# Kernel optimization log

Measured on AMD Instinct MI355X. Metric: run time of the kernel, lower is better.

Reference implementation:

```python
import math
import jax, jax.numpy as jnp
import numpy as np

B, S, D_IN, D_OUT = 8, 4096, 512, 512
CHUNK = 64
MAX_LR = 0.2        # config.max_memory_lr
MIN_DECAY = 0.5     # config.min_memory_decay
MAX_NORM = 30.0     # config.memory_max_norm
NORM_EPS = 1e-5     # config.norm_eps (used in normalize_for_delta)


def setup_inputs() -> dict:
    key = jax.random.key(0)
    ks = jax.random.split(key, 5)
    x = jax.random.normal(ks[0], (B, S, D_IN), dtype=jnp.float32)
    # M_init: xavier_uniform(gain=0.1) ~ small; use small normal
    M_init = jax.random.normal(ks[1], (D_OUT, D_IN), dtype=jnp.float32) * 0.02
    # hyperparam projections (Linear(d_in, 1)); torch init: zero weight, logit bias.
    # Use small random weights so the data-dependent path is exercised.
    eta_w = jax.random.normal(ks[2], (1, D_IN), dtype=jnp.float32) * 0.01
    eta_b = jnp.full((1,), math.log(0.08 / 0.92), dtype=jnp.float32)   # inv_sig(memory_lr_init)
    alpha_w = jax.random.normal(ks[3], (1, D_IN), dtype=jnp.float32) * 0.01
    alpha_b = jnp.full((1,), math.log(0.85 / 0.15), dtype=jnp.float32)  # inv_sig(memory_decay_init)
    gate_w = jax.random.normal(ks[4], (1, D_IN), dtype=jnp.float32) * 0.01
    gate_b = jnp.full((1,), 2.0, dtype=jnp.float32)
    return {"x": x, "M_init": M_init, "eta_w": eta_w, "eta_b": eta_b,
            "alpha_w": alpha_w, "alpha_b": alpha_b, "gate_w": gate_w, "gate_b": gate_b}


def _forward(x, M_init, eta_w, eta_b, alpha_w, alpha_b, gate_w, gate_b):
    n_chunks = S // CHUNK
    # [n_chunks, B, C, d_in] for scan over chunks
    xc = x.reshape(B, n_chunks, CHUNK, D_IN).transpose(1, 0, 2, 3)
    M0 = jnp.broadcast_to(M_init, (B, D_OUT, D_IN))

    def step(M, chunk):  # M: [B, d_out, d_in], chunk: [B, C, d_in]
        # per-chunk hyperparams (training mode: base logits = 0)
        eta_tok = jax.nn.sigmoid(chunk @ eta_w.T + eta_b) * MAX_LR            # [B,C,1]
        alpha_tok = MIN_DECAY + jax.nn.sigmoid(chunk @ alpha_w.T + alpha_b) * (1.0 - MIN_DECAY)
        eta = eta_tok.mean(axis=1, keepdims=True)    # [B,1,1]
        alpha = alpha_tok.mean(axis=1, keepdims=True)
        # retrieval: chunk @ M^T
        outputs = jnp.einsum('bcd,bod->bco', chunk, M)  # [B,C,d_out]
        # normalized keys (F.normalize: x / max(||x||, eps))
        kn = jnp.linalg.norm(chunk, axis=-1, keepdims=True)
        keys = chunk / jnp.maximum(kn, NORM_EPS)
        k_mean = keys.mean(axis=1)        # [B,d_in]
        v_target = outputs.mean(axis=1)   # [B,d_out]
        # delta rule rank-1 update
        Mk = jnp.einsum('bod,bd->bo', M, k_mean)
        error = v_target - Mk
        update = error[:, :, None] * k_mean[:, None, :]  # [B,d_out,d_in]
        # chunk_scale = min(C/chunk_size, 1) = 1 here
        M_new = alpha * M + eta * update
        gate = jax.nn.sigmoid(k_mean @ gate_w.T + gate_b)[:, :, None]  # [B,1,1]
        M_new = gate * M_new + (1.0 - gate) * M
        # frobenius-norm clamp
        M_norm = jnp.sqrt(jnp.sum(M_new * M_new, axis=(-2, -1), keepdims=True))
        scale = jnp.minimum(MAX_NORM / (M_norm + 1e-6), 1.0)
        return M_new * scale, outputs

    M_fin, outs = jax.lax.scan(step, M0, xc)  # outs: [n_chunks,B,C,d_out]
    out = outs.transpose(1, 0, 2, 3).reshape(B, S, D_OUT)
    return out, M_fin


def reference(x, M_init, eta_w, eta_b, alpha_w, alpha_b, gate_w, gate_b):
    return _forward(x, M_init, eta_w, eta_b, alpha_w, alpha_b, gate_w, gate_b)
```

## Files before the change

### kernel.cpp

```cpp
#include <hip/hip_runtime.h>
#include <math.h>

#define DIN  512
#define DOUT 512
#define CHK  64
#define NCH  64
#define NB   8
#define SEQ  4096

typedef short bh8_t __attribute__((ext_vector_type(8)));
typedef float f32x4 __attribute__((ext_vector_type(4)));

__device__ __forceinline__ float sigmoidf_(float z){ return 1.0f/(1.0f+__expf(-z)); }

__device__ __forceinline__ unsigned short f2bf(float f){
  unsigned u = __float_as_uint(f);
  unsigned r = (u + 0x7fffu + ((u>>16)&1u)) >> 16;
  return (unsigned short)r;
}
__device__ __forceinline__ void store_bf4(unsigned short* p, float4 v){
  uint2 u;
  u.x = (unsigned)f2bf(v.x) | ((unsigned)f2bf(v.y)<<16);
  u.y = (unsigned)f2bf(v.z) | ((unsigned)f2bf(v.w)<<16);
  *(uint2*)p = u;
}

__global__ __launch_bounds__(256) void k0_m0h(const float* __restrict__ M0, unsigned short* __restrict__ M0h){
  int idx = (blockIdx.x*256 + threadIdx.x)*4;
  float4 v = *(const float4*)(M0+idx);
  store_bf4(M0h+idx, v);
}

__global__ __launch_bounds__(256) void k1_stats(
    const float* __restrict__ x,
    const float* __restrict__ eta_w, const float* __restrict__ eta_b,
    const float* __restrict__ alpha_w, const float* __restrict__ alpha_b,
    const float* __restrict__ gate_w, const float* __restrict__ gate_b,
    float* __restrict__ KM, float* __restrict__ Dv, unsigned short* __restrict__ KMh,
    float* __restrict__ C1, float* __restrict__ C2, float* __restrict__ KM2, float* __restrict__ Q,
    unsigned short* __restrict__ xh)
{
  int j = blockIdx.x, b = blockIdx.y;
  const float* xc = x + ((size_t)b*SEQ + (size_t)j*CHK) * DIN;
  int tid = threadIdx.x;
  int wave = tid >> 6, lane = tid & 63;

  float km_acc[8], xb_acc[8];
#pragma unroll
  for (int k=0;k<8;k++){ km_acc[k]=0.f; xb_acc[k]=0.f; }
  float eta_sum = 0.f, alpha_sum = 0.f;
  float ew[8], aw[8];
#pragma unroll
  for (int k=0;k<8;k++){ ew[k]=eta_w[lane*8+k]; aw[k]=alpha_w[lane*8+k]; }

  for (int tt=0; tt<16; tt++){
    int t = wave*16 + tt;
    const float* xr = xc + (size_t)t*DIN + lane*8;
    float v[8];
#pragma unroll
    for (int k=0;k<8;k++) v[k]=xr[k];
    if (xh){
      uint4 hv;
      hv.x = (unsigned)f2bf(v[0]) | ((unsigned)f2bf(v[1])<<16);
      hv.y = (unsigned)f2bf(v[2]) | ((unsigned)f2bf(v[3])<<16);
      hv.z = (unsigned)f2bf(v[4]) | ((unsigned)f2bf(v[5])<<16);
      hv.w = (unsigned)f2bf(v[6]) | ((unsigned)f2bf(v[7])<<16);
      *(uint4*)&xh[((size_t)b*SEQ + (size_t)j*CHK + t)*DIN + lane*8] = hv;
    }
    float pe=0.f, pa=0.f, pn=0.f;
#pragma unroll
    for (int k=0;k<8;k++){ pe += v[k]*ew[k]; pa += v[k]*aw[k]; pn += v[k]*v[k]; }
#pragma unroll
    for (int off=32; off; off>>=1){
      pe += __shfl_xor(pe, off);
      pa += __shfl_xor(pa, off);
      pn += __shfl_xor(pn, off);
    }
    float inv = 1.0f / fmaxf(sqrtf(pn), 1e-5f);
    eta_sum   += sigmoidf_(pe + eta_b[0]);
    alpha_sum += sigmoidf_(pa + alpha_b[0]);
#pragma unroll
    for (int k=0;k<8;k++){ km_acc[k] += v[k]*inv; xb_acc[k] += v[k]; }
  }

  __shared__ float sKM[4][DIN];
  __shared__ float sXB[4][DIN];
  __shared__ float sEA[4][2];
  __shared__ float sred[4][2];
#pragma unroll
  for (int k=0;k<8;k++){ sKM[wave][lane*8+k]=km_acc[k]; sXB[wave][lane*8+k]=xb_acc[k]; }
  if (lane==0){ sEA[wave][0]=eta_sum; sEA[wave][1]=alpha_sum; }
  __syncthreads();

  float gpart=0.f, km2part=0.f;
  float kmv[2], dvv[2];
#pragma unroll
  for (int k=0;k<2;k++){
    int d = tid*2+k;
    float km = (sKM[0][d]+sKM[1][d]+sKM[2][d]+sKM[3][d]) * (1.0f/64.0f);
    float xb = (sXB[0][d]+sXB[1][d]+sXB[2][d]+sXB[3][d]) * (1.0f/64.0f);
    kmv[k]=km; dvv[k]=xb-km;
    gpart  += km * gate_w[d];
    km2part+= km * km;
  }
#pragma unroll
  for (int off=32; off; off>>=1){
    gpart   += __shfl_xor(gpart, off);
    km2part += __shfl_xor(km2part, off);
  }
  if (lane==0){ sred[wave][0]=gpart; sred[wave][1]=km2part; }
  __syncthreads();

  size_t base = ((size_t)b*NCH + j)*DIN;
#pragma unroll
  for (int k=0;k<2;k++){
    int d = tid*2+k;
    KM[base+d]=kmv[k];
    Dv[base+d]=dvv[k];
    KMh[base+d]=f2bf(kmv[k]);
  }
  if (tid==0){
    float gdot = sred[0][0]+sred[1][0]+sred[2][0]+sred[3][0];
    float km2  = sred[0][1]+sred[1][1]+sred[2][1]+sred[3][1];
    float etam = (sEA[0][0]+sEA[1][0]+sEA[2][0]+sEA[3][0]) * (1.0f/64.0f);
    float alpm = (sEA[0][1]+sEA[1][1]+sEA[2][1]+sEA[3][1]) * (1.0f/64.0f);
    float eta   = 0.2f * etam;
    float alpha = 0.5f + 0.5f * alpm;
    float gate  = sigmoidf_(gdot + gate_b[0]);
    float c1 = gate*alpha + 1.0f - gate;
    float c2 = gate*eta;
    C1[b*NCH+j]  = c1;
    C2[b*NCH+j]  = c2;
    KM2[b*NCH+j] = km2;
    Q[b*NCH+j]   = c2/c1;
  }
}

__global__ __launch_bounds__(256) void k2_g0h0(
    const float* __restrict__ KM, const float* __restrict__ Dv,
    const float* __restrict__ M0, float* __restrict__ G0, float* __restrict__ H0)
{
  int j = blockIdx.x, b = blockIdx.y, half = blockIdx.z;
  __shared__ float sD[DIN], sK[DIN];
  int tid = threadIdx.x;
  size_t base = ((size_t)b*NCH+j)*DIN;
  for (int d=tid; d<DIN; d+=256){ sD[d]=Dv[base+d]; sK[d]=KM[base+d]; }
  __syncthreads();
  int o = half*256 + tid;
  const float* mr = M0 + (size_t)o*DIN;
  float ag=0.f, ah=0.f;
  for (int d=0; d<DIN; d+=4){
    float4 m = *(const float4*)(mr+d);
    ag += m.x*sD[d] + m.y*sD[d+1] + m.z*sD[d+2] + m.w*sD[d+3];
    ah += m.x*sK[d] + m.y*sK[d+1] + m.z*sK[d+2] + m.w*sK[d+3];
  }
  G0[base+o]=ag; H0[base+o]=ah;
}

__global__ __launch_bounds__(512) void k2b_gram(
    const float* __restrict__ KM, const float* __restrict__ Dv,
    const float* __restrict__ Q,
    float* __restrict__ GT, float* __restrict__ WT)
{
  int i = blockIdx.x, b = blockIdx.y;
  __shared__ float sKi[DIN];
  int tid = threadIdx.x;
  const float* kmi = KM + ((size_t)b*NCH+i)*DIN;
  for (int d=tid; d<DIN; d+=512) sKi[d]=kmi[d];
  __syncthreads();
  float qi = Q[b*NCH+i];
  int wave = tid>>6, lane = tid&63;
  for (int j=wave; j<NCH; j+=8){
    const float* dj = Dv + ((size_t)b*NCH+j)*DIN;
    const float* kj = KM + ((size_t)b*NCH+j)*DIN;
    float pd=0.f, pk=0.f;
#pragma unroll
    for (int k=0;k<8;k++){
      int d = lane + k*64;
      pd += sKi[d]*dj[d];
      pk += sKi[d]*kj[d];
    }
#pragma unroll
    for (int off=32; off; off>>=1){ pd += __shfl_xor(pd,off); pk += __shfl_xor(pk,off); }
    if (lane==0){
      GT[((size_t)b*NCH+j)*NCH + i] = qi*pd;
      WT[((size_t)b*NCH+j)*NCH + i] = qi*pk;
    }
  }
}

__global__ __launch_bounds__(64) void k3a_rec(
    const float* __restrict__ G0, const float* __restrict__ H0,
    const float* __restrict__ GT, const float* __restrict__ WT,
    const float* __restrict__ Q,
    float* __restrict__ AU, unsigned short* __restrict__ UQTh, float* __restrict__ DOTS)
{
  int dblk = blockIdx.x, b = blockIdx.y;
  int lane = threadIdx.x;
  int d = dblk*64 + lane;

  __shared__ float sMT[NCH*NCH];
  __shared__ float sWT[NCH*NCH];
  __shared__ float sq[NCH];

  const float4* gt4 = (const float4*)&GT[(size_t)b*NCH*NCH];
  const float4* wt4 = (const float4*)&WT[(size_t)b*NCH*NCH];
#pragma unroll
  for (int t=0;t<16;t++){
    int idx4 = t*64 + lane;
    int idx  = idx4*4;
    int j = idx>>6, i0 = idx&63;
    float4 g = gt4[idx4];
    float4 w = wt4[idx4];
    if (i0+0 >= j){ g.x=0.f; w.x=0.f; }
    if (i0+1 >= j){ g.y=0.f; w.y=0.f; }
    if (i0+2 >= j){ g.z=0.f; w.z=0.f; }
    if (i0+3 >= j){ g.w=0.f; w.w=0.f; }
    *(float4*)&sMT[idx] = g;
    *(float4*)&sWT[idx] = w;
  }
  sq[lane] = Q[b*NCH+lane];
  __syncthreads();

  float au[NCH];
  size_t gb = (size_t)b*NCH*DOUT + d;
#pragma unroll
  for (int j=0;j<NCH;j++) au[j] = G0[gb + (size_t)j*DOUT];

#pragma unroll
  for (int j=1;j<NCH;j++){
    float a = au[j];
    const f32x4* row = (const f32x4*)&sMT[j*64];
    int ng = (j+3)>>2;
#pragma unroll
    for (int g=0; g<ng; g++){
      f32x4 c = row[g];
      a += c[0]*au[g*4+0] + c[1]*au[g*4+1] + c[2]*au[g*4+2] + c[3]*au[g*4+3];
    }
    au[j] = a;
  }
#pragma unroll
  for (int j=0;j<NCH;j++) AU[gb + (size_t)j*DOUT] = au[j];

#pragma unroll
  for (int g=0; g<8; g++){
    uint4 hv;
    hv.x = (unsigned)f2bf(au[g*8+0]*sq[g*8+0]) | ((unsigned)f2bf(au[g*8+1]*sq[g*8+1])<<16);
    hv.y = (unsigned)f2bf(au[g*8+2]*sq[g*8+2]) | ((unsigned)f2bf(au[g*8+3]*sq[g*8+3])<<16);
    hv.z = (unsigned)f2bf(au[g*8+4]*sq[g*8+4]) | ((unsigned)f2bf(au[g*8+5]*sq[g*8+5])<<16);
    hv.w = (unsigned)f2bf(au[g*8+6]*sq[g*8+6]) | ((unsigned)f2bf(au[g*8+7]*sq[g*8+7])<<16);
    *(uint4*)&UQTh[((size_t)b*DOUT + d)*NCH + g*8] = hv;
  }

#pragma unroll
  for (int j=0;j<NCH;j++){
    float w = H0[gb + (size_t)j*DOUT];
    const f32x4* row = (const f32x4*)&sWT[j*64];
    int ng = (j+3)>>2;
#pragma unroll
    for (int g=0; g<ng; g++){
      f32x4 c = row[g];
      w += c[0]*au[g*4+0] + c[1]*au[g*4+1] + c[2]*au[g*4+2] + c[3]*au[g*4+3];
    }
    float s1 = au[j]*w, s2 = au[j]*au[j];
#pragma unroll
    for (int off=32; off; off>>=1){ s1+=__shfl_xor(s1,off); s2+=__shfl_xor(s2,off); }
    if (lane==0){
      DOTS[(((size_t)b*8+dblk)*NCH+j)*2+0] = s1;
      DOTS[(((size_t)b*8+dblk)*NCH+j)*2+1] = s2;
    }
  }
}

__global__ __launch_bounds__(256) void k3b_chain(
    const float* __restrict__ M0, const float* __restrict__ DOTS,
    const float* __restrict__ C1, const float* __restrict__ C2, const float* __restrict__ KM2,
    float* __restrict__ P)
{
  int b = blockIdx.x;
  int tid = threadIdx.x, wave = tid>>6, lane = tid&63;
  __shared__ float sF[4];
  __shared__ float suw[NCH], suu[NCH], sc1[NCH], sc2[NCH], skm2[NCH];

  float f0p = 0.f;
  const float4* m4 = (const float4*)M0;
  for (int i=tid; i<(DOUT*DIN)/4; i+=256){
    float4 v = m4[i];
    f0p += v.x*v.x + v.y*v.y + v.z*v.z + v.w*v.w;
  }
#pragma unroll
  for (int off=32; off; off>>=1) f0p += __shfl_xor(f0p, off);
  if (lane==0) sF[wave]=f0p;

  if (tid < NCH){
    float uw=0.f, uu=0.f;
#pragma unroll
    for (int k=0;k<8;k++){
      uw += DOTS[(((size_t)b*8+k)*NCH+tid)*2+0];
      uu += DOTS[(((size_t)b*8+k)*NCH+tid)*2+1];
    }
    suw[tid]=uw; suu[tid]=uu;
    sc1[tid]=C1[b*NCH+tid]; sc2[tid]=C2[b*NCH+tid]; skm2[tid]=KM2[b*NCH+tid];
  }
  __syncthreads();

  if (tid==0){
    float F = sF[0]+sF[1]+sF[2]+sF[3];
    float p = 1.f;
    P[b*65+0] = 1.f;
    for (int j=0;j<NCH;j++){
      float uw = suw[j], uu = suu[j];
      float c1 = sc1[j], c2 = sc2[j], km2 = skm2[j];
      uw *= p*p; uu *= p*p;
      float Fnew = c1*c1*F + 2.f*c1*c2*uw + c2*c2*uu*km2;
      float scale = fminf(30.0f/(sqrtf(Fnew)+1e-6f), 1.0f);
      F = scale*scale*Fnew;
      p = scale*c1*p;
      P[b*65+j+1] = p;
    }
  }
}

__global__ __launch_bounds__(256) void k4s_s(
    const float* __restrict__ x, const unsigned short* __restrict__ xh,
    const unsigned short* __restrict__ KMh,
    unsigned short* __restrict__ Sh, int use_xh)
{
  int tt = blockIdx.x, b = blockIdx.y;
  int tid = threadIdx.x;
  int lane = tid&63, w = tid>>6, m = lane&15, q = lane>>4;
  __shared__ unsigned short As[64*72];
  __shared__ unsigned short Bs[64*72];
  f32x4 acc[4];
  f32x4 z = {0.f,0.f,0.f,0.f};
#pragma unroll
  for (int nf=0;nf<4;nf++) acc[nf]=z;

  for (int k0=0;k0<DIN;k0+=64){
    uint4 bb[2];
#pragma unroll
    for (int v=0;v<2;v++){
      int idx=v*256+tid; int il=idx>>3, cc=idx&7;
      bb[v] = *(const uint4*)&KMh[((size_t)b*NCH+il)*DIN + k0 + cc*8];
    }
    if (use_xh){
      uint4 av[2];
#pragma unroll
      for (int v=0;v<2;v++){
        int idx=v*256+tid; int row=idx>>3, cc=idx&7;
        av[v] = *(const uint4*)&xh[((size_t)b*SEQ + (size_t)tt*64 + row)*DIN + k0 + cc*8];
      }
      __syncthreads();
#pragma unroll
      for (int v=0;v<2;v++){
        int idx=v*256+tid; int row=idx>>3, cc=idx&7;
        *(uint4*)&As[row*72 + cc*8] = av[v];
      }
    } else {
      float4 xa[4];
#pragma unroll
      for (int v=0;v<4;v++){
        int idx=v*256+tid; int row=idx>>4, cc=idx&15;
        xa[v] = *(const float4*)(x + ((size_t)b*SEQ + (size_t)tt*64 + row)*DIN + k0 + cc*4);
      }
      __syncthreads();
#pragma unroll
      for (int v=0;v<4;v++){
        int idx=v*256+tid; int row=idx>>4, cc=idx&15;
        store_bf4(&As[row*72 + cc*4], xa[v]);
      }
    }
#pragma unroll
    for (int v=0;v<2;v++){
      int idx=v*256+tid; int il=idx>>3, cc=idx&7;
      *(uint4*)&Bs[il*72 + cc*8] = bb[v];
    }
    __syncthreads();
#pragma unroll
    for (int kk=0;kk<2;kk++){
      bh8_t af = *(bh8_t*)&As[(w*16+m)*72 + kk*32 + q*8];
#pragma unroll
      for (int nf=0;nf<4;nf++){
        bh8_t bf_ = *(bh8_t*)&Bs[(nf*16+m)*72 + kk*32 + q*8];
        acc[nf] = __builtin_amdgcn_mfma_f32_16x16x32_bf16(af, bf_, acc[nf], 0,0,0);
      }
    }
  }
  __syncthreads();
  unsigned short* tb = As + w*16*72;
#pragma unroll
  for (int nf=0;nf<4;nf++)
#pragma unroll
    for (int r=0;r<4;r++)
      tb[(q*4+r)*72 + nf*16 + m] = f2bf(acc[nf][r]);
#pragma unroll
  for (int v=0;v<2;v++){
    int idx = v*64 + lane;
    int row = idx>>3, c8 = idx&7;
    uint4 vv = *(uint4*)&tb[row*72 + c8*8];
    *(uint4*)&Sh[((size_t)b*SEQ + (size_t)tt*64 + w*16 + row)*NCH + c8*8] = vv;
  }
}

#define ASTRIDE 80
__global__ __launch_bounds__(512, 4) void k4_out(
    const float* __restrict__ x, const unsigned short* __restrict__ xh,
    const unsigned short* __restrict__ M0h,
    const unsigned short* __restrict__ Sh, const unsigned short* __restrict__ UQTh,
    const float* __restrict__ P, float* __restrict__ out, int use_xh)
{
  int n = blockIdx.x;
  int xcd = n & 7, local = n >> 3;
  int work = xcd*64 + local;
  int ot = work & 3, rb = (work>>2) & 15, b = work >> 6;

  int tid = threadIdx.x;
  int lane = tid&63, w = tid>>6, m = lane&15, q = lane>>4;
  int wr = w>>1, wc = w&1;
  int O0 = ot*128;
  int R0 = rb*256;

  __shared__ __align__(16) char pool[(256+128)*ASTRIDE*2];
  unsigned short* As = (unsigned short*)pool;
  unsigned short* Bs = (unsigned short*)pool + 256*ASTRIDE;
  float* ep = (float*)pool;

  f32x4 acc[4][4];
  f32x4 z = {0.f,0.f,0.f,0.f};
#pragma unroll
  for (int mi=0;mi<4;mi++)
#pragma unroll
    for (int nf=0;nf<4;nf++) acc[mi][nf]=z;

#pragma unroll
  for (int v=0; v<4; v++){
    int idx = v*512 + tid;
    int row = idx>>3, cc = idx&7;
    int j = (R0 + row)>>6;
    uint4 sv = *(const uint4*)&Sh[((size_t)b*SEQ + R0 + row)*NCH + cc*8];
    int i0 = cc*8;
    unsigned m0 = (i0+0 < j) ? ((i0+1 < j)?0xFFFFFFFFu:0x0000FFFFu) : 0u;
    unsigned m1 = (i0+2 < j) ? ((i0+3 < j)?0xFFFFFFFFu:0x0000FFFFu) : 0u;
    unsigned m2 = (i0+4 < j) ? ((i0+5 < j)?0xFFFFFFFFu:0x0000FFFFu) : 0u;
    unsigned m3 = (i0+6 < j) ? ((i0+7 < j)?0xFFFFFFFFu:0x0000FFFFu) : 0u;
    sv.x&=m0; sv.y&=m1; sv.z&=m2; sv.w&=m3;
    *(uint4*)&As[row*ASTRIDE + cc*8] = sv;
  }
#pragma unroll
  for (int v=0; v<2; v++){
    int idx = v*512 + tid;
    int ol = idx>>3, cc = idx&7;
    *(uint4*)&Bs[ol*ASTRIDE + cc*8] = *(const uint4*)&UQTh[((size_t)b*DOUT + O0+ol)*NCH + cc*8];
  }

  uint4 pB[2], pA[4];
  float4 xa[8];
#pragma unroll
  for (int v=0;v<2;v++){
    int idx=v*512+tid; int ol=idx>>3, cc=idx&7;
    pB[v] = *(const uint4*)&M0h[(size_t)(O0+ol)*DIN + 0 + cc*8];
  }
  if (use_xh){
#pragma unroll
    for (int v=0;v<4;v++){
      int idx=v*512+tid; int row=idx>>3, cc=idx&7;
      pA[v] = *(const uint4*)&xh[((size_t)b*SEQ + R0 + row)*DIN + 0 + cc*8];
    }
  } else {
#pragma unroll
    for (int v=0;v<8;v++){
      int idx=v*512+tid; int row=idx>>4, cc=idx&15;
      xa[v] = *(const float4*)(x + ((size_t)b*SEQ + R0 + row)*DIN + 0 + cc*4);
    }
  }

  __syncthreads();
#pragma unroll
  for (int kk=0;kk<2;kk++){
#pragma unroll
    for (int mi=0;mi<4;mi++){
      bh8_t af = *(bh8_t*)&As[(wr*64+mi*16+m)*ASTRIDE + kk*32 + q*8];
#pragma unroll
      for (int nf=0;nf<4;nf++){
        bh8_t bf_ = *(bh8_t*)&Bs[(wc*64+nf*16+m)*ASTRIDE + kk*32 + q*8];
        acc[mi][nf] = __builtin_amdgcn_mfma_f32_16x16x32_bf16(af, bf_, acc[mi][nf], 0,0,0);
      }
    }
  }

  for (int k0=0;k0<DIN;k0+=64){
    __syncthreads();
#pragma unroll
    for (int v=0;v<2;v++){
      int idx=v*512+tid; int ol=idx>>3, cc=idx&7;
      *(uint4*)&Bs[ol*ASTRIDE + cc*8] = pB[v];
    }
    if (use_xh){
#pragma unroll
      for (int v=0;v<4;v++){
        int idx=v*512+tid; int row=idx>>3, cc=idx&7;
        *(uint4*)&As[row*ASTRIDE + cc*8] = pA[v];
      }
    } else {
#pragma unroll
      for (int v=0;v<8;v++){
        int idx=v*512+tid; int row=idx>>4, cc=idx&15;
        store_bf4(&As[row*ASTRIDE + cc*4], xa[v]);
      }
    }
    int kn = k0 + 64;
    if (kn < DIN){
#pragma unroll
      for (int v=0;v<2;v++){
        int idx=v*512+tid; int ol=idx>>3, cc=idx&7;
        pB[v] = *(const uint4*)&M0h[(size_t)(O0+ol)*DIN + kn + cc*8];
      }
      if (use_xh){
#pragma unroll
        for (int v=0;v<4;v++){
          int idx=v*512+tid; int row=idx>>3, cc=idx&7;
          pA[v] = *(const uint4*)&xh[((size_t)b*SEQ + R0 + row)*DIN + kn + cc*8];
        }
      } else {
#pragma unroll
        for (int v=0;v<8;v++){
          int idx=v*512+tid; int row=idx>>4, cc=idx&15;
          xa[v] = *(const float4*)(x + ((size_t)b*SEQ + R0 + row)*DIN + kn + cc*4);
        }
      }
    }
    __syncthreads();
#pragma unroll
    for (int kk=0;kk<2;kk++){
#pragma unroll
      for (int mi=0;mi<4;mi++){
        bh8_t af = *(bh8_t*)&As[(wr*64+mi*16+m)*ASTRIDE + kk*32 + q*8];
#pragma unroll
        for (int nf=0;nf<4;nf++){
          bh8_t bf_ = *(bh8_t*)&Bs[(wc*64+nf*16+m)*ASTRIDE + kk*32 + q*8];
          acc[mi][nf] = __builtin_amdgcn_mfma_f32_16x16x32_bf16(af, bf_, acc[mi][nf], 0,0,0);
        }
      }
    }
  }

  __syncthreads();
  float p = P[b*65 + rb*4 + wr];
  float* epw = ep + w*(16*68);
#pragma unroll
  for (int mi=0; mi<4; mi++){
#pragma unroll
    for (int nf=0;nf<4;nf++)
#pragma unroll
      for (int r=0;r<4;r++)
        epw[(q*4+r)*68 + nf*16 + m] = p*acc[mi][nf][r];
#pragma unroll
    for (int v=0;v<4;v++){
      int idx = v*64 + lane;
      int row = idx>>4, c4 = idx&15;
      float4 vv = *(float4*)&epw[row*68 + c4*4];
      *(float4*)&out[((size_t)b*SEQ + R0 + wr*64 + mi*16 + row)*DOUT + O0 + wc*64 + c4*4] = vv;
    }
  }
}

__global__ __launch_bounds__(256) void k5_mfin(
    const float* __restrict__ M0, const float* __restrict__ KM,
    const float* __restrict__ AU, const float* __restrict__ P, const float* __restrict__ Q,
    float* __restrict__ Mout)
{
  int ob = blockIdx.x, b = blockIdx.y;
  int tid = threadIdx.x;
  __shared__ float uo[64][8];
  for (int idx=tid; idx<512; idx+=256){
    int i = idx>>3, oo = idx&7;
    uo[i][oo] = Q[b*NCH+i] * AU[((size_t)b*NCH+i)*DOUT + ob*8+oo];
  }
  __syncthreads();
  float p64 = P[b*65+NCH];
  float acc[2][8];
#pragma unroll
  for (int h=0;h<2;h++)
#pragma unroll
    for (int oo=0;oo<8;oo++) acc[h][oo]=0.f;
  int d0 = tid, d1 = tid+256;
  for (int i=0;i<64;i++){
    float k0 = KM[((size_t)b*NCH+i)*DIN + d0];
    float k1 = KM[((size_t)b*NCH+i)*DIN + d1];
#pragma unroll
    for (int oo=0;oo<8;oo++){
      float u = uo[i][oo];
      acc[0][oo] += u*k0;
      acc[1][oo] += u*k1;
    }
  }
#pragma unroll
  for (int oo=0;oo<8;oo++){
    int o = ob*8+oo;
    Mout[((size_t)b*DOUT + o)*DIN + d0] = p64*(M0[(size_t)o*DIN+d0] + acc[0][oo]);
    Mout[((size_t)b*DOUT + o)*DIN + d1] = p64*(M0[(size_t)o*DIN+d1] + acc[1][oo]);
  }
}

extern "C" void kernel_launch(void* const* d_in, const int* in_sizes, int n_in,
                              void* d_out, int out_size, void* d_ws, size_t ws_size,
                              hipStream_t stream) {
  const float* x       = (const float*)d_in[0];
  const float* M0      = (const float*)d_in[1];
  const float* eta_w   = (const float*)d_in[2];
  const float* eta_b   = (const float*)d_in[3];
  const float* alpha_w = (const float*)d_in[4];
  const float* alpha_b = (const float*)d_in[5];
  const float* gate_w  = (const float*)d_in[6];
  const float* gate_b  = (const float*)d_in[7];
  float* out = (float*)d_out;

  float* ws = (float*)d_ws;
  float* KM   = ws;
  float* Dv   = KM   + 262144;
  float* G0   = Dv   + 262144;
  float* H0   = G0   + 262144;
  float* AU   = H0   + 262144;
  float* GT   = AU   + 262144;
  float* WT   = GT   + 32768;
  float* C1   = WT   + 32768;
  float* C2   = C1   + 512;
  float* KM2  = C2   + 512;
  float* Q    = KM2  + 512;
  float* P    = Q    + 512;
  float* DOTS = P    + 1024;
  unsigned short* M0h  = (unsigned short*)(DOTS + 8192);
  unsigned short* KMh  = M0h  + 262144;
  unsigned short* Sh   = KMh  + 262144;
  unsigned short* UQTh = Sh   + 2097152;
  unsigned short* xh   = UQTh + 262144;

  size_t base_bytes = (size_t)((char*)xh - (char*)d_ws);
  size_t need_xh = base_bytes + (size_t)16777216*2;
  int use_xh = (ws_size >= need_xh) ? 1 : 0;
  unsigned short* xh_arg = use_xh ? xh : (unsigned short*)0;

  k0_m0h<<<dim3(256), 256, 0, stream>>>(M0, M0h);
  k1_stats<<<dim3(NCH, NB), 256, 0, stream>>>(x, eta_w, eta_b, alpha_w, alpha_b,
                                              gate_w, gate_b, KM, Dv, KMh, C1, C2, KM2, Q, xh_arg);
  k2_g0h0<<<dim3(NCH, NB, 2), 256, 0, stream>>>(KM, Dv, M0, G0, H0);
  k2b_gram<<<dim3(NCH, NB), 512, 0, stream>>>(KM, Dv, Q, GT, WT);
  k4s_s<<<dim3(SEQ/64, NB), 256, 0, stream>>>(x, xh, KMh, Sh, use_xh);
  k3a_rec<<<dim3(8, NB), 64, 0, stream>>>(G0, H0, GT, WT, Q, AU, UQTh, DOTS);
  k3b_chain<<<dim3(NB), 256, 0, stream>>>(M0, DOTS, C1, C2, KM2, P);
  k4_out<<<dim3(512), 512, 0, stream>>>(x, xh, M0h, Sh, UQTh, P, out, use_xh);
  k5_mfin<<<dim3(64, NB), 256, 0, stream>>>(M0, KM, AU, P, Q, out + (size_t)NB*SEQ*DOUT);
}
```

Before: 476.9 us.

## Retile G0/H0 and S kernels with register prefetch; nontemporal output stores

k2_g0h0 is restructured so each block caches 16 rows of M0 in shared memory and loops over all chunks, instead of each block streaming all of M0 for one chunk. This cuts the repeated global reads of M0. k4s_s now computes 128-row tiles with a 2x2 wave layout, padded LDS stride and register prefetch of the next K slice, which overlaps loads with MFMA. The k4_out epilogue uses nontemporal stores to avoid polluting the cache with the large output. Risks include lower parallelism in k2 (256 blocks) and more register pressure in k4s_s.

```diff
diff --git a/kernel.cpp b/kernel.cpp
--- a/kernel.cpp
+++ b/kernel.cpp
@@ -140,21 +140,36 @@
     const float* __restrict__ KM, const float* __restrict__ Dv,
     const float* __restrict__ M0, float* __restrict__ G0, float* __restrict__ H0)
 {
-  int j = blockIdx.x, b = blockIdx.y, half = blockIdx.z;
-  __shared__ float sD[DIN], sK[DIN];
+  int os = blockIdx.x, b = blockIdx.y;
+  int o0 = os*16;
+  __shared__ float sM0[16*DIN];
   int tid = threadIdx.x;
-  size_t base = ((size_t)b*NCH+j)*DIN;
-  for (int d=tid; d<DIN; d+=256){ sD[d]=Dv[base+d]; sK[d]=KM[base+d]; }
-  __syncthreads();
-  int o = half*256 + tid;
-  const float* mr = M0 + (size_t)o*DIN;
-  float ag=0.f, ah=0.f;
-  for (int d=0; d<DIN; d+=4){
-    float4 m = *(const float4*)(mr+d);
-    ag += m.x*sD[d] + m.y*sD[d+1] + m.z*sD[d+2] + m.w*sD[d+3];
-    ah += m.x*sK[d] + m.y*sK[d+1] + m.z*sK[d+2] + m.w*sK[d+3];
-  }
-  G0[base+o]=ag; H0[base+o]=ah;
+  {
+    const float4* src = (const float4*)(M0 + (size_t)o0*DIN);
+    float4* dst = (float4*)sM0;
+#pragma unroll
+    for (int v=0; v<8; v++) dst[v*256+tid] = src[v*256+tid];
+  }
+  __syncthreads();
+  int o = tid>>4;
+  int ks = tid&15;
+  const float* m0r = sM0 + o*DIN + ks*32;
+  for (int j=0;j<NCH;j++){
+    size_t base = ((size_t)b*NCH+j)*DIN;
+    const float4* kr = (const float4*)(KM + base + ks*32);
+    const float4* dr = (const float4*)(Dv + base + ks*32);
+    float ag=0.f, ah=0.f;
+#pragma unroll
+    for (int t=0;t<8;t++){
+      float4 kv = kr[t], dv = dr[t];
+      const float* mm = m0r + t*4;
+      ah += mm[0]*kv.x + mm[1]*kv.y + mm[2]*kv.z + mm[3]*kv.w;
+      ag += mm[0]*dv.x + mm[1]*dv.y + mm[2]*dv.z + mm[3]*dv.w;
+    }
+#pragma unroll
+    for (int off=8; off; off>>=1){ ag += __shfl_xor(ag,off); ah += __shfl_xor(ah,off); }
+    if (ks==0){ G0[base + o0 + o] = ag; H0[base + o0 + o] = ah; }
+  }
 }
 
 __global__ __launch_bounds__(512) void k2b_gram(
@@ -321,84 +336,117 @@
   }
 }
 
-__global__ __launch_bounds__(256) void k4s_s(
+#define SSTRIDE 80
+__global__ __launch_bounds__(256, 4) void k4s_s(
     const float* __restrict__ x, const unsigned short* __restrict__ xh,
     const unsigned short* __restrict__ KMh,
     unsigned short* __restrict__ Sh, int use_xh)
 {
-  int tt = blockIdx.x, b = blockIdx.y;
+  int rb = blockIdx.x, b = blockIdx.y;
+  int R0 = rb*128;
   int tid = threadIdx.x;
   int lane = tid&63, w = tid>>6, m = lane&15, q = lane>>4;
-  __shared__ unsigned short As[64*72];
-  __shared__ unsigned short Bs[64*72];
-  f32x4 acc[4];
+  int wr = w>>1, wc = w&1;
+
+  __shared__ unsigned short As[128*SSTRIDE];
+  __shared__ unsigned short Bs[64*SSTRIDE];
+
+  f32x4 acc[4][2];
   f32x4 z = {0.f,0.f,0.f,0.f};
 #pragma unroll
-  for (int nf=0;nf<4;nf++) acc[nf]=z;
+  for (int mi=0;mi<4;mi++)
+#pragma unroll
+    for (int nf=0;nf<2;nf++) acc[mi][nf]=z;
+
+  uint4 pB[2], pA[4];
+  float4 xa[8];
+#pragma unroll
+  for (int v=0;v<2;v++){
+    int idx=v*256+tid; int il=idx>>3, cc=idx&7;
+    pB[v] = *(const uint4*)&KMh[((size_t)b*NCH+il)*DIN + 0 + cc*8];
+  }
+  if (use_xh){
+#pragma unroll
+    for (int v=0;v<4;v++){
+      int idx=v*256+tid; int row=idx>>3, cc=idx&7;
+      pA[v] = *(const uint4*)&xh[((size_t)b*SEQ + R0 + row)*DIN + 0 + cc*8];
+    }
+  } else {
+#pragma unroll
+    for (int v=0;v<8;v++){
+      int idx=v*256+tid; int row=idx>>4, cc=idx&15;
+      xa[v] = *(const float4*)(x + ((size_t)b*SEQ + R0 + row)*DIN + 0 + cc*4);
+    }
+  }
 
   for (int k0=0;k0<DIN;k0+=64){
-    uint4 bb[2];
+    __syncthreads();
 #pragma unroll
     for (int v=0;v<2;v++){
       int idx=v*256+tid; int il=idx>>3, cc=idx&7;
-      bb[v] = *(const uint4*)&KMh[((size_t)b*NCH+il)*DIN + k0 + cc*8];
+      *(uint4*)&Bs[il*SSTRIDE + cc*8] = pB[v];
     }
     if (use_xh){
-      uint4 av[2];
+#pragma unroll
+      for (int v=0;v<4;v++){
+        int idx=v*256+tid; int row=idx>>3, cc=idx&7;
+        *(uint4*)&As[row*SSTRIDE + cc*8] = pA[v];
+      }
+    } else {
+#pragma unroll
+      for (int v=0;v<8;v++){
+        int idx=v*256+tid; int row=idx>>4, cc=idx&15;
+        store_bf4(&As[row*SSTRIDE + cc*4], xa[v]);
+      }
+    }
+    int kn = k0 + 64;
+    if (kn < DIN){
 #pragma unroll
       for (int v=0;v<2;v++){
-        int idx=v*256+tid; int row=idx>>3, cc=idx&7;
-        av[v] = *(const uint4*)&xh[((size_t)b*SEQ + (size_t)tt*64 + row)*DIN + k0 + cc*8];
-      }
-      __syncthreads();
-#pragma unroll
-      for (int v=0;v<2;v++){
-        int idx=v*256+tid; int row=idx>>3, cc=idx&7;
-        *(uint4*)&As[row*72 + cc*8] = av[v];
-      }
-    } else {
-      float4 xa[4];
-#pragma unroll
-      for (int v=0;v<4;v++){
-        int idx=v*256+tid; int row=idx>>4, cc=idx&15;
-        xa[v] = *(const float4*)(x + ((size_t)b*SEQ + (size_t)tt*64 + row)*DIN + k0 + cc*4);
-      }
-      __syncthreads();
-#pragma unroll
-      for (int v=0;v<4;v++){
-        int idx=v*256+tid; int row=idx>>4, cc=idx&15;
-        store_bf4(&As[row*72 + cc*4], xa[v]);
-      }
-    }
-#pragma unroll
-    for (int v=0;v<2;v++){
-      int idx=v*256+tid; int il=idx>>3, cc=idx&7;
-      *(uint4*)&Bs[il*72 + cc*8] = bb[v];
+        int idx=v*256+tid; int il=idx>>3, cc=idx&7;
+        pB[v] = *(const uint4*)&KMh[((size_t)b*NCH+il)*DIN + kn + cc*8];
+      }
+      if (use_xh){
+#pragma unroll
+        for (int v=0;v<4;v++){
+          int idx=v*256+tid; int row=idx>>3, cc=idx&7;
+          pA[v] = *(const uint4*)&xh[((size_t)b*SEQ + R0 + row)*DIN + kn + cc*8];
+        }
+      } else {
+#pragma unroll
+        for (int v=0;v<8;v++){
+          int idx=v*256+tid; int row=idx>>4, cc=idx&15;
+          xa[v] = *(const float4*)(x + ((size_t)b*SEQ + R0 + row)*DIN + kn + cc*4);
+        }
+      }
     }
     __syncthreads();
 #pragma unroll
     for (int kk=0;kk<2;kk++){
-      bh8_t af = *(bh8_t*)&As[(w*16+m)*72 + kk*32 + q*8];
-#pragma unroll
-      for (int nf=0;nf<4;nf++){
-        bh8_t bf_ = *(bh8_t*)&Bs[(nf*16+m)*72 + kk*32 + q*8];
-        acc[nf] = __builtin_amdgcn_mfma_f32_16x16x32_bf16(af, bf_, acc[nf], 0,0,0);
-      }
-    }
-  }
-  __syncthreads();
-  unsigned short* tb = As + w*16*72;
-#pragma unroll
-  for (int nf=0;nf<4;nf++)
-#pragma unroll
-    for (int r=0;r<4;r++)
-      tb[(q*4+r)*72 + nf*16 + m] = f2bf(acc[nf][r]);
-#pragma unroll
-  for (int v=0;v<2;v++){
-    int idx = v*64 + lane;
-    int row = idx>>3, c8 = idx&7;
-    uint4 vv = *(uint4*)&tb[row*72 + c8*8];
-    *(uint4*)&Sh[((size_t)b*SEQ + (size_t)tt*64 + w*16 + row)*NCH + c8*8] = vv;
+#pragma unroll
+      for (int mi=0;mi<4;mi++){
+        bh8_t af = *(bh8_t*)&As[(wr*64+mi*16+m)*SSTRIDE + kk*32 + q*8];
+#pragma unroll
+        for (int nf=0;nf<2;nf++){
+          bh8_t bf_ = *(bh8_t*)&Bs[(wc*32+nf*16+m)*SSTRIDE + kk*32 + q*8];
+          acc[mi][nf] = __builtin_amdgcn_mfma_f32_16x16x32_bf16(af, bf_, acc[mi][nf], 0,0,0);
+        }
+      }
+    }
+  }
+
+  __syncthreads();
+  unsigned short* tb = As + w*16*40;
+#pragma unroll
+  for (int mi=0; mi<4; mi++){
+#pragma unroll
+    for (int nf=0;nf<2;nf++)
+#pragma unroll
+      for (int r=0;r<4;r++)
+        tb[(q*4+r)*40 + nf*16 + m] = f2bf(acc[mi][nf][r]);
+    int row = lane>>2, c8 = lane&3;
+    uint4 vv = *(uint4*)&tb[row*40 + c8*8];
+    *(uint4*)&Sh[((size_t)b*SEQ + R0 + wr*64 + mi*16 + row)*NCH + wc*32 + c8*8] = vv;
   }
 }
 
@@ -558,8 +606,9 @@
     for (int v=0;v<4;v++){
       int idx = v*64 + lane;
       int row = idx>>4, c4 = idx&15;
-      float4 vv = *(float4*)&epw[row*68 + c4*4];
-      *(float4*)&out[((size_t)b*SEQ + R0 + wr*64 + mi*16 + row)*DOUT + O0 + wc*64 + c4*4] = vv;
+      f32x4 vv = *(f32x4*)&epw[row*68 + c4*4];
+      f32x4* pdst = (f32x4*)&out[((size_t)b*SEQ + R0 + wr*64 + mi*16 + row)*DOUT + O0 + wc*64 + c4*4];
+      __builtin_nontemporal_store(vv, pdst);
     }
   }
 }
@@ -643,9 +692,9 @@
   k0_m0h<<<dim3(256), 256, 0, stream>>>(M0, M0h);
   k1_stats<<<dim3(NCH, NB), 256, 0, stream>>>(x, eta_w, eta_b, alpha_w, alpha_b,
                                               gate_w, gate_b, KM, Dv, KMh, C1, C2, KM2, Q, xh_arg);
-  k2_g0h0<<<dim3(NCH, NB, 2), 256, 0, stream>>>(KM, Dv, M0, G0, H0);
+  k2_g0h0<<<dim3(32, NB), 256, 0, stream>>>(KM, Dv, M0, G0, H0);
   k2b_gram<<<dim3(NCH, NB), 512, 0, stream>>>(KM, Dv, Q, GT, WT);
-  k4s_s<<<dim3(SEQ/64, NB), 256, 0, stream>>>(x, xh, KMh, Sh, use_xh);
+  k4s_s<<<dim3(SEQ/128, NB), 256, 0, stream>>>(x, xh, KMh, Sh, use_xh);
   k3a_rec<<<dim3(8, NB), 64, 0, stream>>>(G0, H0, GT, WT, Q, AU, UQTh, DOTS);
   k3b_chain<<<dim3(NB), 256, 0, stream>>>(M0, DOTS, C1, C2, KM2, P);
   k4_out<<<dim3(512), 512, 0, stream>>>(x, xh, M0h, Sh, UQTh, P, out, use_xh);
```

After: 525.0 us. 1.1x slower.

## Fuse S=x·KM^T computation into output kernel, drop separate k4s_s pass

Applied to the files above, without the earlier changes.

Removes the separate kernel that computed S = x·KM^T into a bf16 global buffer. The output GEMM kernel now also loads KM tiles alongside M0 and accumulates S in extra MFMA accumulators while it streams x. After the main loop it masks S causally, writes it to LDS and does the UQT correction GEMM. This saves a second full read of x, the S write/read round trip and one launch. In exchange each output block recomputes S redundantly across its four output tiles, and the kernel needs more registers and LDS. Output stores also become nontemporal.

```diff
diff --git a/kernel.cpp b/kernel.cpp
--- a/kernel.cpp
+++ b/kernel.cpp
@@ -321,92 +321,11 @@
   }
 }
 
-__global__ __launch_bounds__(256) void k4s_s(
-    const float* __restrict__ x, const unsigned short* __restrict__ xh,
-    const unsigned short* __restrict__ KMh,
-    unsigned short* __restrict__ Sh, int use_xh)
-{
-  int tt = blockIdx.x, b = blockIdx.y;
-  int tid = threadIdx.x;
-  int lane = tid&63, w = tid>>6, m = lane&15, q = lane>>4;
-  __shared__ unsigned short As[64*72];
-  __shared__ unsigned short Bs[64*72];
-  f32x4 acc[4];
-  f32x4 z = {0.f,0.f,0.f,0.f};
-#pragma unroll
-  for (int nf=0;nf<4;nf++) acc[nf]=z;
-
-  for (int k0=0;k0<DIN;k0+=64){
-    uint4 bb[2];
-#pragma unroll
-    for (int v=0;v<2;v++){
-      int idx=v*256+tid; int il=idx>>3, cc=idx&7;
-      bb[v] = *(const uint4*)&KMh[((size_t)b*NCH+il)*DIN + k0 + cc*8];
-    }
-    if (use_xh){
-      uint4 av[2];
-#pragma unroll
-      for (int v=0;v<2;v++){
-        int idx=v*256+tid; int row=idx>>3, cc=idx&7;
-        av[v] = *(const uint4*)&xh[((size_t)b*SEQ + (size_t)tt*64 + row)*DIN + k0 + cc*8];
-      }
-      __syncthreads();
-#pragma unroll
-      for (int v=0;v<2;v++){
-        int idx=v*256+tid; int row=idx>>3, cc=idx&7;
-        *(uint4*)&As[row*72 + cc*8] = av[v];
-      }
-    } else {
-      float4 xa[4];
-#pragma unroll
-      for (int v=0;v<4;v++){
-        int idx=v*256+tid; int row=idx>>4, cc=idx&15;
-        xa[v] = *(const float4*)(x + ((size_t)b*SEQ + (size_t)tt*64 + row)*DIN + k0 + cc*4);
-      }
-      __syncthreads();
-#pragma unroll
-      for (int v=0;v<4;v++){
-        int idx=v*256+tid; int row=idx>>4, cc=idx&15;
-        store_bf4(&As[row*72 + cc*4], xa[v]);
-      }
-    }
-#pragma unroll
-    for (int v=0;v<2;v++){
-      int idx=v*256+tid; int il=idx>>3, cc=idx&7;
-      *(uint4*)&Bs[il*72 + cc*8] = bb[v];
-    }
-    __syncthreads();
-#pragma unroll
-    for (int kk=0;kk<2;kk++){
-      bh8_t af = *(bh8_t*)&As[(w*16+m)*72 + kk*32 + q*8];
-#pragma unroll
-      for (int nf=0;nf<4;nf++){
-        bh8_t bf_ = *(bh8_t*)&Bs[(nf*16+m)*72 + kk*32 + q*8];
-        acc[nf] = __builtin_amdgcn_mfma_f32_16x16x32_bf16(af, bf_, acc[nf], 0,0,0);
-      }
-    }
-  }
-  __syncthreads();
-  unsigned short* tb = As + w*16*72;
-#pragma unroll
-  for (int nf=0;nf<4;nf++)
-#pragma unroll
-    for (int r=0;r<4;r++)
-      tb[(q*4+r)*72 + nf*16 + m] = f2bf(acc[nf][r]);
-#pragma unroll
-  for (int v=0;v<2;v++){
-    int idx = v*64 + lane;
-    int row = idx>>3, c8 = idx&7;
-    uint4 vv = *(uint4*)&tb[row*72 + c8*8];
-    *(uint4*)&Sh[((size_t)b*SEQ + (size_t)tt*64 + w*16 + row)*NCH + c8*8] = vv;
-  }
-}
-
 #define ASTRIDE 80
 __global__ __launch_bounds__(512, 4) void k4_out(
     const float* __restrict__ x, const unsigned short* __restrict__ xh,
-    const unsigned short* __restrict__ M0h,
-    const unsigned short* __restrict__ Sh, const unsigned short* __restrict__ UQTh,
+    const unsigned short* __restrict__ M0h, const unsigned short* __restrict__ KMh,
+    const unsigned short* __restrict__ UQTh,
     const float* __restrict__ P, float* __restrict__ out, int use_xh)
 {
   int n = blockIdx.x;
@@ -420,45 +339,32 @@
   int O0 = ot*128;
   int R0 = rb*256;
 
-  __shared__ __align__(16) char pool[(256+128)*ASTRIDE*2];
+  __shared__ __align__(16) char pool[(256+192)*ASTRIDE*2];
   unsigned short* As = (unsigned short*)pool;
   unsigned short* Bs = (unsigned short*)pool + 256*ASTRIDE;
   float* ep = (float*)pool;
 
   f32x4 acc[4][4];
+  f32x4 accS[4][2];
   f32x4 z = {0.f,0.f,0.f,0.f};
 #pragma unroll
-  for (int mi=0;mi<4;mi++)
+  for (int mi=0;mi<4;mi++){
 #pragma unroll
     for (int nf=0;nf<4;nf++) acc[mi][nf]=z;
-
-#pragma unroll
-  for (int v=0; v<4; v++){
-    int idx = v*512 + tid;
-    int row = idx>>3, cc = idx&7;
-    int j = (R0 + row)>>6;
-    uint4 sv = *(const uint4*)&Sh[((size_t)b*SEQ + R0 + row)*NCH + cc*8];
-    int i0 = cc*8;
-    unsigned m0 = (i0+0 < j) ? ((i0+1 < j)?0xFFFFFFFFu:0x0000FFFFu) : 0u;
-    unsigned m1 = (i0+2 < j) ? ((i0+3 < j)?0xFFFFFFFFu:0x0000FFFFu) : 0u;
-    unsigned m2 = (i0+4 < j) ? ((i0+5 < j)?0xFFFFFFFFu:0x0000FFFFu) : 0u;
-    unsigned m3 = (i0+6 < j) ? ((i0+7 < j)?0xFFFFFFFFu:0x0000FFFFu) : 0u;
-    sv.x&=m0; sv.y&=m1; sv.z&=m2; sv.w&=m3;
-    *(uint4*)&As[row*ASTRIDE + cc*8] = sv;
-  }
-#pragma unroll
-  for (int v=0; v<2; v++){
-    int idx = v*512 + tid;
-    int ol = idx>>3, cc = idx&7;
-    *(uint4*)&Bs[ol*ASTRIDE + cc*8] = *(const uint4*)&UQTh[((size_t)b*DOUT + O0+ol)*NCH + cc*8];
-  }
-
-  uint4 pB[2], pA[4];
+#pragma unroll
+    for (int sf=0;sf<2;sf++) accS[mi][sf]=z;
+  }
+
+  uint4 pBM[2], pBK, pA[4];
   float4 xa[8];
 #pragma unroll
   for (int v=0;v<2;v++){
     int idx=v*512+tid; int ol=idx>>3, cc=idx&7;
-    pB[v] = *(const uint4*)&M0h[(size_t)(O0+ol)*DIN + 0 + cc*8];
+    pBM[v] = *(const uint4*)&M0h[(size_t)(O0+ol)*DIN + 0 + cc*8];
+  }
+  {
+    int il = tid>>3, cc = tid&7;
+    pBK = *(const uint4*)&KMh[((size_t)b*NCH+il)*DIN + 0 + cc*8];
   }
   if (use_xh){
 #pragma unroll
@@ -474,26 +380,16 @@
     }
   }
 
-  __syncthreads();
-#pragma unroll
-  for (int kk=0;kk<2;kk++){
-#pragma unroll
-    for (int mi=0;mi<4;mi++){
-      bh8_t af = *(bh8_t*)&As[(wr*64+mi*16+m)*ASTRIDE + kk*32 + q*8];
-#pragma unroll
-      for (int nf=0;nf<4;nf++){
-        bh8_t bf_ = *(bh8_t*)&Bs[(wc*64+nf*16+m)*ASTRIDE + kk*32 + q*8];
-        acc[mi][nf] = __builtin_amdgcn_mfma_f32_16x16x32_bf16(af, bf_, acc[mi][nf], 0,0,0);
-      }
-    }
-  }
-
   for (int k0=0;k0<DIN;k0+=64){
     __syncthreads();
 #pragma unroll
     for (int v=0;v<2;v++){
       int idx=v*512+tid; int ol=idx>>3, cc=idx&7;
-      *(uint4*)&Bs[ol*ASTRIDE + cc*8] = pB[v];
+      *(uint4*)&Bs[ol*ASTRIDE + cc*8] = pBM[v];
+    }
+    {
+      int il = tid>>3, cc = tid&7;
+      *(uint4*)&Bs[(128+il)*ASTRIDE + cc*8] = pBK;
     }
     if (use_xh){
 #pragma unroll
@@ -513,7 +409,11 @@
 #pragma unroll
       for (int v=0;v<2;v++){
         int idx=v*512+tid; int ol=idx>>3, cc=idx&7;
-        pB[v] = *(const uint4*)&M0h[(size_t)(O0+ol)*DIN + kn + cc*8];
+        pBM[v] = *(const uint4*)&M0h[(size_t)(O0+ol)*DIN + kn + cc*8];
+      }
+      {
+        int il = tid>>3, cc = tid&7;
+        pBK = *(const uint4*)&KMh[((size_t)b*NCH+il)*DIN + kn + cc*8];
       }
       if (use_xh){
 #pragma unroll
@@ -540,6 +440,46 @@
           bh8_t bf_ = *(bh8_t*)&Bs[(wc*64+nf*16+m)*ASTRIDE + kk*32 + q*8];
           acc[mi][nf] = __builtin_amdgcn_mfma_f32_16x16x32_bf16(af, bf_, acc[mi][nf], 0,0,0);
         }
+#pragma unroll
+        for (int sf=0;sf<2;sf++){
+          bh8_t bs_ = *(bh8_t*)&Bs[(128+wc*32+sf*16+m)*ASTRIDE + kk*32 + q*8];
+          accS[mi][sf] = __builtin_amdgcn_mfma_f32_16x16x32_bf16(af, bs_, accS[mi][sf], 0,0,0);
+        }
+      }
+    }
+  }
+
+  __syncthreads();
+#pragma unroll
+  for (int v=0; v<2; v++){
+    int idx = v*512 + tid;
+    int ol = idx>>3, cc = idx&7;
+    *(uint4*)&Bs[ol*ASTRIDE + cc*8] = *(const uint4*)&UQTh[((size_t)b*DOUT + O0+ol)*NCH + cc*8];
+  }
+#pragma unroll
+  for (int mi=0;mi<4;mi++){
+#pragma unroll
+    for (int sf=0;sf<2;sf++){
+      int i = wc*32 + sf*16 + m;
+#pragma unroll
+      for (int r=0;r<4;r++){
+        int rloc = wr*64 + mi*16 + q*4 + r;
+        int j = (R0 + rloc)>>6;
+        unsigned short hv = (i < j) ? f2bf(accS[mi][sf][r]) : (unsigned short)0;
+        As[rloc*ASTRIDE + i] = hv;
+      }
+    }
+  }
+  __syncthreads();
+#pragma unroll
+  for (int kk=0;kk<2;kk++){
+#pragma unroll
+    for (int mi=0;mi<4;mi++){
+      bh8_t af = *(bh8_t*)&As[(wr*64+mi*16+m)*ASTRIDE + kk*32 + q*8];
+#pragma unroll
+      for (int nf=0;nf<4;nf++){
+        bh8_t bf_ = *(bh8_t*)&Bs[(wc*64+nf*16+m)*ASTRIDE + kk*32 + q*8];
+        acc[mi][nf] = __builtin_amdgcn_mfma_f32_16x16x32_bf16(af, bf_, acc[mi][nf], 0,0,0);
       }
     }
   }
@@ -558,8 +498,9 @@
     for (int v=0;v<4;v++){
       int idx = v*64 + lane;
       int row = idx>>4, c4 = idx&15;
-      float4 vv = *(float4*)&epw[row*68 + c4*4];
-      *(float4*)&out[((size_t)b*SEQ + R0 + wr*64 + mi*16 + row)*DOUT + O0 + wc*64 + c4*4] = vv;
+      f32x4 vv = *(f32x4*)&epw[row*68 + c4*4];
+      f32x4* pdst = (f32x4*)&out[((size_t)b*SEQ + R0 + wr*64 + mi*16 + row)*DOUT + O0 + wc*64 + c4*4];
+      __builtin_nontemporal_store(vv, pdst);
     }
   }
 }
@@ -645,9 +586,8 @@
                                               gate_w, gate_b, KM, Dv, KMh, C1, C2, KM2, Q, xh_arg);
   k2_g0h0<<<dim3(NCH, NB, 2), 256, 0, stream>>>(KM, Dv, M0, G0, H0);
   k2b_gram<<<dim3(NCH, NB), 512, 0, stream>>>(KM, Dv, Q, GT, WT);
-  k4s_s<<<dim3(SEQ/64, NB), 256, 0, stream>>>(x, xh, KMh, Sh, use_xh);
   k3a_rec<<<dim3(8, NB), 64, 0, stream>>>(G0, H0, GT, WT, Q, AU, UQTh, DOTS);
   k3b_chain<<<dim3(NB), 256, 0, stream>>>(M0, DOTS, C1, C2, KM2, P);
-  k4_out<<<dim3(512), 512, 0, stream>>>(x, xh, M0h, Sh, UQTh, P, out, use_xh);
+  k4_out<<<dim3(512), 512, 0, stream>>>(x, xh, M0h, KMh, UQTh, P, out, use_xh);
   k5_mfin<<<dim3(64, NB), 256, 0, stream>>>(M0, KM, AU, P, Q, out + (size_t)NB*SEQ*DOUT);
 }
```

Result: slower. 550.7 us (+15.5%).
